# Kernel tuning notes

Measured on AMD Instinct MI355X. Metric: run time of the kernel, lower is better.

## Reference

```python
import jax, jax.numpy as jnp
import numpy as np


def _cost_volume(l_fmap, r_fmap, max_disp):
    # l_fmap, r_fmap: [N, C, H, W]. cost[n,d,h,w] = mean_c l[n,c,h,w] * r[n,c,h,w-d]
    # for w >= d, else 0. Both the naive and conv2d torch variants compute this.
    w = l_fmap.shape[-1]
    items = []
    for d in range(max_disp):
        # mean over channel dim of shifted product -> [N, H, W-d]
        item = jnp.mean(l_fmap[:, :, :, d:] * r_fmap[:, :, :, : w - d], axis=1)
        # left-pad along width with zeros back to W
        items.append(jnp.pad(item, ((0, 0), (0, 0), (d, 0))))
    return jnp.stack(items, axis=1)  # [N, max_disp, H, W]


def setup_inputs() -> dict:
    key = jax.random.key(0)
    k1, k2 = jax.random.split(key)
    N, C, H, W = 8, 32, 256, 512
    return {
        "l_fmap": jax.random.normal(k1, (N, C, H, W), dtype=jnp.float32),
        "r_fmap": jax.random.normal(k2, (N, C, H, W), dtype=jnp.float32),
        "use_naive": 1,
        "max_disp": 64,
    }


def reference(l_fmap, r_fmap, use_naive, max_disp):
    # use_naive only selects between two mathematically identical torch paths;
    # the computed cost volume is the same either way.
    return _cost_volume(l_fmap, r_fmap, max_disp)
```

## Files before the change

kernel.cpp:

```cpp
#include <hip/hip_runtime.h>

#define NB 8
#define CC 32
#define HH 256
#define WW 512
#define DD 64
#define PAD 64
#define RPITCH (WW + PAD)
#define CHUNK 8
#define NCHUNK (CC / CHUNK)

__global__ __launch_bounds__(512) void cost_volume_kernel(
    const float* __restrict__ L, const float* __restrict__ R, float* __restrict__ O)
{
    __shared__ float lA[CHUNK * WW];
    __shared__ float rB[CHUNK * RPITCH];

    const int tid = threadIdx.x;
    const int row = blockIdx.x;
    const int n = row >> 8;
    const int h = row & 255;
    const size_t inbase = (size_t)n * (CC * HH * WW) + (size_t)h * WW;

    if (tid < CHUNK * 16) {
        const int c = tid >> 4, q = tid & 15;
        *reinterpret_cast<float4*>(&rB[c * RPITCH + q * 4]) =
            make_float4(0.f, 0.f, 0.f, 0.f);
    }

    const int wave = tid >> 6, lane = tid & 63;
    const int d0 = (wave & 3) * 16;
    const int cw = ((wave >> 2) << 6) + lane;
    const int w0 = cw * 4;
    const int rbase = PAD + w0 - d0 - 16;

    float acc[16][4];
    #pragma unroll
    for (int dd = 0; dd < 16; ++dd)
        #pragma unroll
        for (int j = 0; j < 4; ++j) acc[dd][j] = 0.f;

    float4 lr0, lr1, rr0, rr1;
    const int f0 = tid, c_0 = f0 >> 7, q_0 = f0 & 127;
    const int f1 = tid + 512, c_1 = f1 >> 7, q_1 = f1 & 127;

    auto ld = [&](int ch) {
        const int c0 = ch * CHUNK;
        const size_t g0 = inbase + (size_t)(c0 + c_0) * (HH * WW);
        const size_t g1 = inbase + (size_t)(c0 + c_1) * (HH * WW);
        lr0 = reinterpret_cast<const float4*>(L + g0)[q_0];
        rr0 = reinterpret_cast<const float4*>(R + g0)[q_0];
        lr1 = reinterpret_cast<const float4*>(L + g1)[q_1];
        rr1 = reinterpret_cast<const float4*>(R + g1)[q_1];
    };

    ld(0);

    for (int ch = 0; ch < NCHUNK; ++ch) {
        __syncthreads();

        *reinterpret_cast<float4*>(&lA[c_0 * WW + q_0 * 4]) = lr0;
        *reinterpret_cast<float4*>(&rB[c_0 * RPITCH + PAD + q_0 * 4]) = rr0;
        *reinterpret_cast<float4*>(&lA[c_1 * WW + q_1 * 4]) = lr1;
        *reinterpret_cast<float4*>(&rB[c_1 * RPITCH + PAD + q_1 * 4]) = rr1;

        if (ch + 1 < NCHUNK) ld(ch + 1);

        __syncthreads();

        #pragma unroll
        for (int c = 0; c < CHUNK; ++c) {
            const float4 lv = *reinterpret_cast<const float4*>(&lA[c * WW + w0]);
            float rwin[20];
            #pragma unroll
            for (int k = 0; k < 5; ++k) {
                const float4 rv = *reinterpret_cast<const float4*>(&rB[c * RPITCH + rbase + k * 4]);
                rwin[k * 4 + 0] = rv.x; rwin[k * 4 + 1] = rv.y;
                rwin[k * 4 + 2] = rv.z; rwin[k * 4 + 3] = rv.w;
            }
            const float lvv[4] = {lv.x, lv.y, lv.z, lv.w};
            #pragma unroll
            for (int dd = 0; dd < 16; ++dd)
                #pragma unroll
                for (int j = 0; j < 4; ++j)
                    acc[dd][j] = fmaf(lvv[j], rwin[16 + j - dd], acc[dd][j]);
        }
    }

    const float inv = 1.0f / 32.0f;
    const size_t obase = (size_t)n * ((size_t)DD * HH * WW) + (size_t)h * WW + w0;
    #pragma unroll
    for (int dd = 0; dd < 16; ++dd) {
        float4 o;
        o.x = acc[dd][0] * inv; o.y = acc[dd][1] * inv;
        o.z = acc[dd][2] * inv; o.w = acc[dd][3] * inv;
        *reinterpret_cast<float4*>(&O[obase + (size_t)(d0 + dd) * (HH * WW)]) = o;
    }
}

extern "C" void kernel_launch(void* const* d_in, const int* in_sizes, int n_in,
                              void* d_out, int out_size, void* d_ws, size_t ws_size,
                              hipStream_t stream) {
    const float* L = (const float*)d_in[0];
    const float* R = (const float*)d_in[1];
    float* O = (float*)d_out;
    cost_volume_kernel<<<NB * HH, 512, 0, stream>>>(L, R, O);
}
```

Before: 135.3 us.

## Split each image row across two blocks with halo loads and larger channel chunks

Each block now handles half a row (256 columns) with 256 threads instead of a full row with 512 threads, doubling the grid. The second half loads a 64-column halo of R from the preceding columns, and the first half zero-fills it. Channel chunks grow from 8 to 16 so there are two pipeline stages instead of four, and launch bounds request 4 blocks per CU. The aim is better occupancy and load balance at the cost of redundant halo traffic and more registers for staged loads.

```diff
diff --git a/kernel.cpp b/kernel.cpp
--- a/kernel.cpp
+++ b/kernel.cpp
@@ -1,38 +1,40 @@
 #include <hip/hip_runtime.h>
 
-#define NB 8
 #define CC 32
 #define HH 256
 #define WW 512
 #define DD 64
-#define PAD 64
-#define RPITCH (WW + PAD)
-#define CHUNK 8
+#define WB 256
+#define PRE 64
+#define RT (WB + PRE)
+#define CHUNK 16
 #define NCHUNK (CC / CHUNK)
 
-__global__ __launch_bounds__(512) void cost_volume_kernel(
+__global__ __launch_bounds__(256, 4) void cost_volume_kernel(
     const float* __restrict__ L, const float* __restrict__ R, float* __restrict__ O)
 {
-    __shared__ float lA[CHUNK * WW];
-    __shared__ float rB[CHUNK * RPITCH];
+    __shared__ float lA[CHUNK * WB];
+    __shared__ float rB[CHUNK * RT];
 
     const int tid = threadIdx.x;
-    const int row = blockIdx.x;
+    const int bid = blockIdx.x;
+    const int half = bid & 1;
+    const int row = bid >> 1;
     const int n = row >> 8;
     const int h = row & 255;
-    const size_t inbase = (size_t)n * (CC * HH * WW) + (size_t)h * WW;
+    const int wstart = half * WB;
+    const size_t inbase = (size_t)n * (CC * HH * WW) + (size_t)h * WW + wstart;
 
-    if (tid < CHUNK * 16) {
+    if (half == 0) {
         const int c = tid >> 4, q = tid & 15;
-        *reinterpret_cast<float4*>(&rB[c * RPITCH + q * 4]) =
+        *reinterpret_cast<float4*>(&rB[c * RT + q * 4]) =
             make_float4(0.f, 0.f, 0.f, 0.f);
     }
 
     const int wave = tid >> 6, lane = tid & 63;
-    const int d0 = (wave & 3) * 16;
-    const int cw = ((wave >> 2) << 6) + lane;
-    const int w0 = cw * 4;
-    const int rbase = PAD + w0 - d0 - 16;
+    const int d0 = wave * 16;
+    const int w0 = lane * 4;
+    const int rbase = PRE + w0 - d0 - 16;
 
     float acc[16][4];
     #pragma unroll
@@ -40,18 +42,43 @@
         #pragma unroll
         for (int j = 0; j < 4; ++j) acc[dd][j] = 0.f;
 
-    float4 lr0, lr1, rr0, rr1;
-    const int f0 = tid, c_0 = f0 >> 7, q_0 = f0 & 127;
-    const int f1 = tid + 512, c_1 = f1 >> 7, q_1 = f1 & 127;
+    float4 lr0, lr1, lr2, lr3, rr0, rr1, rr2, rr3, pr;
+    const int c_0 = (tid          ) >> 6, q_0 = (tid          ) & 63;
+    const int c_1 = (tid + 256    ) >> 6, q_1 = (tid + 256    ) & 63;
+    const int c_2 = (tid + 512    ) >> 6, q_2 = (tid + 512    ) & 63;
+    const int c_3 = (tid + 768    ) >> 6, q_3 = (tid + 768    ) & 63;
+    const int cp  = tid >> 4,             qp  = tid & 15;
 
     auto ld = [&](int ch) {
         const int c0 = ch * CHUNK;
         const size_t g0 = inbase + (size_t)(c0 + c_0) * (HH * WW);
         const size_t g1 = inbase + (size_t)(c0 + c_1) * (HH * WW);
+        const size_t g2 = inbase + (size_t)(c0 + c_2) * (HH * WW);
+        const size_t g3 = inbase + (size_t)(c0 + c_3) * (HH * WW);
         lr0 = reinterpret_cast<const float4*>(L + g0)[q_0];
         rr0 = reinterpret_cast<const float4*>(R + g0)[q_0];
         lr1 = reinterpret_cast<const float4*>(L + g1)[q_1];
         rr1 = reinterpret_cast<const float4*>(R + g1)[q_1];
+        lr2 = reinterpret_cast<const float4*>(L + g2)[q_2];
+        rr2 = reinterpret_cast<const float4*>(R + g2)[q_2];
+        lr3 = reinterpret_cast<const float4*>(L + g3)[q_3];
+        rr3 = reinterpret_cast<const float4*>(R + g3)[q_3];
+        if (half == 1) {
+            const size_t gp = inbase + (size_t)(c0 + cp) * (HH * WW) - PRE;
+            pr = reinterpret_cast<const float4*>(R + gp)[qp];
+        }
+    };
+    auto wr = [&]() {
+        *reinterpret_cast<float4*>(&lA[c_0 * WB + q_0 * 4]) = lr0;
+        *reinterpret_cast<float4*>(&rB[c_0 * RT + PRE + q_0 * 4]) = rr0;
+        *reinterpret_cast<float4*>(&lA[c_1 * WB + q_1 * 4]) = lr1;
+        *reinterpret_cast<float4*>(&rB[c_1 * RT + PRE + q_1 * 4]) = rr1;
+        *reinterpret_cast<float4*>(&lA[c_2 * WB + q_2 * 4]) = lr2;
+        *reinterpret_cast<float4*>(&rB[c_2 * RT + PRE + q_2 * 4]) = rr2;
+        *reinterpret_cast<float4*>(&lA[c_3 * WB + q_3 * 4]) = lr3;
+        *reinterpret_cast<float4*>(&rB[c_3 * RT + PRE + q_3 * 4]) = rr3;
+        if (half == 1)
+            *reinterpret_cast<float4*>(&rB[cp * RT + qp * 4]) = pr;
     };
 
     ld(0);
@@ -59,22 +86,18 @@
     for (int ch = 0; ch < NCHUNK; ++ch) {
         __syncthreads();
 
-        *reinterpret_cast<float4*>(&lA[c_0 * WW + q_0 * 4]) = lr0;
-        *reinterpret_cast<float4*>(&rB[c_0 * RPITCH + PAD + q_0 * 4]) = rr0;
-        *reinterpret_cast<float4*>(&lA[c_1 * WW + q_1 * 4]) = lr1;
-        *reinterpret_cast<float4*>(&rB[c_1 * RPITCH + PAD + q_1 * 4]) = rr1;
-
+        wr();
         if (ch + 1 < NCHUNK) ld(ch + 1);
 
         __syncthreads();
 
-        #pragma unroll
+        #pragma unroll 4
         for (int c = 0; c < CHUNK; ++c) {
-            const float4 lv = *reinterpret_cast<const float4*>(&lA[c * WW + w0]);
+            const float4 lv = *reinterpret_cast<const float4*>(&lA[c * WB + w0]);
             float rwin[20];
             #pragma unroll
             for (int k = 0; k < 5; ++k) {
-                const float4 rv = *reinterpret_cast<const float4*>(&rB[c * RPITCH + rbase + k * 4]);
+                const float4 rv = *reinterpret_cast<const float4*>(&rB[c * RT + rbase + k * 4]);
                 rwin[k * 4 + 0] = rv.x; rwin[k * 4 + 1] = rv.y;
                 rwin[k * 4 + 2] = rv.z; rwin[k * 4 + 3] = rv.w;
             }
@@ -88,7 +111,8 @@
     }
 
     const float inv = 1.0f / 32.0f;
-    const size_t obase = (size_t)n * ((size_t)DD * HH * WW) + (size_t)h * WW + w0;
+    const size_t obase = (size_t)n * ((size_t)DD * HH * WW) + (size_t)h * WW
+                       + wstart + w0;
     #pragma unroll
     for (int dd = 0; dd < 16; ++dd) {
         float4 o;
@@ -104,5 +128,5 @@
     const float* L = (const float*)d_in[0];
     const float* R = (const float*)d_in[1];
     float* O = (float*)d_out;
-    cost_volume_kernel<<<NB * HH, 512, 0, stream>>>(L, R, O);
+    cost_volume_kernel<<<8 * HH * 2, 256, 0, stream>>>(L, R, O);
 }
```

Result: slower. 261.3 us (+93.2%).
